# Performance work log

Hardware: AMD Instinct MI355X
Metric: run time of the kernel (lower is better)

## Reference

```python
import jax, jax.numpy as jnp
import numpy as np

NUM_HEADS = 8
SCALE_BASE = 512.0
GN_EPS = 1e-5


def rotate_every_two(x):
    x1 = x[..., ::2]
    x2 = x[..., 1::2]
    return jnp.stack([-x2, x1], axis=-1).reshape(x.shape)


def xpos_apply(x, downscale):
    # x: [B, T, D]; XPOS rotary with length-dependent scale (offset=0)
    L, D = x.shape[1], x.shape[2]
    half = D // 2
    scale_vec = (jnp.arange(0, D, 2, dtype=jnp.float32) + 0.4 * D) / (1.4 * D)  # [half]
    pos = jnp.arange(L, dtype=jnp.float32)
    scale = scale_vec[None, :] ** (pos[:, None] / SCALE_BASE)  # [L, half]
    inv_freq = 1.0 / (10000.0 ** (jnp.arange(half, dtype=jnp.float32) / half))
    sinusoid = pos[:, None] * inv_freq[None, :]  # [L, half]
    sin, cos = jnp.sin(sinusoid), jnp.cos(sinusoid)
    if downscale:
        scale = 1.0 / scale
    sin_s = jnp.repeat(sin * scale, 2, axis=-1)  # duplicate_interleave -> [L, D]
    cos_s = jnp.repeat(cos * scale, 2, axis=-1)
    return x * cos_s + rotate_every_two(x) * sin_s


def decay_mask_fn(T, num_heads):
    # gamma per head; decay stored as log(gamma) so mask = gamma^(i-j) on lower triangle
    s, e = np.log(1.0 / 32.0), np.log(1.0 / 512.0)
    gamma = 1.0 - jnp.exp(jnp.linspace(s, e, num_heads).astype(jnp.float32))
    log_decay = jnp.log(gamma)  # [H], negative
    idx = jnp.arange(T)
    expo = (idx[:, None] - idx[None, :]).astype(jnp.float32)  # i - j
    tri = (idx[:, None] >= idx[None, :])
    expo_safe = jnp.where(tri, expo, 0.0)
    mask = jnp.exp(log_decay[:, None, None] * expo_safe) * tri  # [H, T, T]
    scale = jnp.sqrt(mask.sum(axis=-1, keepdims=True))  # [H, T, 1]
    return mask / scale


def setup_inputs() -> dict:
    key = jax.random.key(0)
    ks = jax.random.split(key, 4)
    B, T, E = 2, 2048, 1024
    V = 2 * E
    return {
        "hidden_states": jax.random.normal(ks[0], (B, T, E), dtype=jnp.float32),
        "w_qkv": jax.random.normal(ks[1], (E, 2 * E + V), dtype=jnp.float32) * 0.02,
        "b_qkv": jnp.zeros((2 * E + V,), dtype=jnp.float32),
        "w_g": jax.random.normal(ks[2], (E, V), dtype=jnp.float32) * 0.02,
        "b_g": jnp.zeros((V,), dtype=jnp.float32),
        "w_p": jax.random.normal(ks[3], (V, E), dtype=jnp.float32) * 0.02,
        "b_p": jnp.zeros((E,), dtype=jnp.float32),
    }


def reference(hidden_states, w_qkv, b_qkv, w_g, b_g, w_p, b_p):
    B, T, E = hidden_states.shape
    H = NUM_HEADS
    V = 2 * E
    dk, dv = E // H, V // H

    qkv = hidden_states @ w_qkv + b_qkv
    q, k, v = qkv[..., :E], qkv[..., E:2 * E], qkv[..., 2 * E:]
    q = xpos_apply(q, downscale=False)
    k = xpos_apply(k, downscale=True)

    # split heads -> [B, H, T, d]
    q = q.reshape(B, T, H, dk).transpose(0, 2, 1, 3)
    k = k.reshape(B, T, H, dk).transpose(0, 2, 1, 3)
    v = v.reshape(B, T, H, dv).transpose(0, 2, 1, 3)

    mask = decay_mask_fn(T, H)  # [H, T, T]

    # parallel retention
    retention = jnp.einsum("bhid,bhjd->bhij", q, k) * (dk ** -0.5)
    retention = retention * mask[None]  # [B, H, T, T]
    out = jnp.einsum("bhij,bhjv->bhiv", retention, v)

    # current_kv = sum_j mask[h, -1, j] * k_j (x) v_j
    curr_kv = jnp.einsum("hj,bhjk,bhjv->bhkv", mask[:, -1, :], k, v)

    retention_out = out.transpose(0, 2, 1, 3).reshape(B, T, V)

    # GroupNorm(num_groups=H, affine=False) over v_dim channels
    g = retention_out.reshape(B * T, H, dv)
    mu = g.mean(axis=-1, keepdims=True)
    var = ((g - mu) ** 2).mean(axis=-1, keepdims=True)
    normed = ((g - mu) / jnp.sqrt(var + GN_EPS)).reshape(B, T, V)

    gated = jax.nn.silu(hidden_states @ w_g + b_g) * normed
    proj = gated @ w_p + b_p
    return proj, curr_kv
```

## Files before the change

### kernel.cpp

```cpp
#include <hip/hip_runtime.h>
#include <math.h>

#define BT      4096
#define T_SEQ   2048
#define E_DIM   1024
#define V_DIM   2048
#define DK      128
#define DV      256

typedef unsigned short ushort_t;
typedef __attribute__((ext_vector_type(8)))  short bf16x8;
typedef __attribute__((ext_vector_type(4)))  unsigned short u16x4;
typedef __attribute__((ext_vector_type(16))) float f32x16;

__device__ __forceinline__ void decay_params(int h, float& ld, float& gamma) {
    const float s0 = -3.4657359027997265f;
    const float e0 = -6.2383246250395092f;
    float lin = s0 + (e0 - s0) * ((float)h * (1.0f / 7.0f));
    gamma = 1.0f - expf(lin);
    ld = logf(gamma);
}

__device__ __forceinline__ short f2bf(float f) {
    unsigned u = __float_as_uint(f);
    unsigned r = (u + 0x7fffu + ((u >> 16) & 1u)) >> 16;
    return (short)r;
}
__device__ __forceinline__ float bf2f(ushort_t u) {
    return __uint_as_float((unsigned)u << 16);
}

__device__ __forceinline__ void async_copy16(void* lds, const void* g) {
    __builtin_amdgcn_global_load_lds(
        (const __attribute__((address_space(1))) unsigned int*)g,
        (__attribute__((address_space(3))) unsigned int*)lds, 16, 0, 0);
}

__device__ __forceinline__ void xcd_tile(int& bx, int& by) {
    const int nwgx = gridDim.x;
    const int nwg  = nwgx * gridDim.y;
    int bid = blockIdx.y * nwgx + blockIdx.x;
    bid = (bid & 7) * (nwg >> 3) + (bid >> 3);
    bx = bid % nwgx;
    by = bid / nwgx;
}

__device__ __forceinline__ void xcd_map_qkv(int& bx, int& by) {
    int bid = blockIdx.y * 16 + blockIdx.x;
    const int xcd = bid & 7, idx = bid >> 3;
    bx = (xcd & 1) * 8 + (idx & 7);
    by = (xcd >> 1) * 4 + (idx >> 3);
}

__device__ __forceinline__ void xcd_map_gate(int& bx, int& by) {
    int bid = blockIdx.y * 8 + blockIdx.x;
    const int xcd = bid & 7, idx = bid >> 3;
    bx = (xcd & 1) * 4 + (idx & 3);
    by = (xcd >> 1) * 8 + (idx >> 2);
}

__device__ __forceinline__ void transpose_tile_body(
    const float* __restrict__ W, ushort_t* __restrict__ Wt,
    int K, int N, int bx, int by, float (*tile)[33], int t)
{
    const int k0 = by * 32, n0 = bx * 32;
    const int r = t >> 3, c = (t & 7) * 4;
    float4 v = *(const float4*)&W[(size_t)(k0 + r) * N + n0 + c];
    tile[r][c] = v.x; tile[r][c + 1] = v.y; tile[r][c + 2] = v.z; tile[r][c + 3] = v.w;
    __syncthreads();
    u16x4 o;
    o[0] = (ushort_t)f2bf(tile[c][r]);
    o[1] = (ushort_t)f2bf(tile[c + 1][r]);
    o[2] = (ushort_t)f2bf(tile[c + 2][r]);
    o[3] = (ushort_t)f2bf(tile[c + 3][r]);
    *(u16x4*)&Wt[(size_t)(n0 + r) * K + k0 + c] = o;
}

__global__ __launch_bounds__(256)
void prep_batch(const float* __restrict__ hs, ushort_t* __restrict__ hs_bf,
                const float* __restrict__ w_qkv, ushort_t* __restrict__ wqkv_t,
                const float* __restrict__ w_g, ushort_t* __restrict__ wg_t)
{
    __shared__ float tile[32][33];
    const int t = threadIdx.x;
    const int blk = blockIdx.x;
    if (blk < 4096) {
        transpose_tile_body(w_qkv, wqkv_t, 1024, 4096, blk % 128, blk / 128, tile, t);
    } else if (blk < 6144) {
        const int u = blk - 4096;
        transpose_tile_body(w_g, wg_t, 1024, 2048, u % 64, u / 64, tile, t);
    } else {
        const int u = blk - 6144;
        int i = (u * 256 + t) * 8;
        float4 a = *(const float4*)&hs[i];
        float4 b = *(const float4*)&hs[i + 4];
        bf16x8 o;
        o[0] = f2bf(a.x); o[1] = f2bf(a.y); o[2] = f2bf(a.z); o[3] = f2bf(a.w);
        o[4] = f2bf(b.x); o[5] = f2bf(b.y); o[6] = f2bf(b.z); o[7] = f2bf(b.w);
        *(bf16x8*)&hs_bf[i] = o;
    }
}

__global__ __launch_bounds__(256)
void transpose_w_kernel(const float* __restrict__ W, ushort_t* __restrict__ Wt,
                        int K, int N)
{
    __shared__ float tile[32][33];
    transpose_tile_body(W, Wt, K, N, blockIdx.x, blockIdx.y, tile, threadIdx.x);
}

__global__ __launch_bounds__(512, 2)
void gemm256p8(const ushort_t* __restrict__ A,
               const ushort_t* __restrict__ Bt,
               const float* __restrict__ bias,
               ushort_t* __restrict__ C, int ldc, int nkt)
{
    __shared__ ushort_t As[2 * 16384];
    __shared__ ushort_t Bs[2 * 16384];

    const int tid = threadIdx.x;
    const int wid = tid >> 6, l = tid & 63;
    const int lc = l & 31, q = l >> 5;
    const int wr = wid >> 2, wc = wid & 3;
    int bx, by; xcd_map_qkv(bx, by);
    const int m0 = by * 256, n0 = bx * 256;

    const int sra = tid >> 3;
    const int spa = (tid & 7) ^ (sra & 7);
    const ushort_t* gA = A + (size_t)(m0 + sra) * 1024 + spa * 8;
    const int srb = tid >> 2;
    const int spb = (tid & 3) ^ ((srb >> 1) & 3);
    const ushort_t* gB = Bt + (size_t)(n0 + srb) * 1024 + spb * 8;
    const int da = tid * 8;

    int arow0 = (wr * 128 +  0 + lc) * 64;
    int arow1 = (wr * 128 + 32 + lc) * 64;
    int arow2 = (wr * 128 + 64 + lc) * 64;
    int arow3 = (wr * 128 + 96 + lc) * 64;
    int sk0 = ((0 * 2 + q) ^ (lc & 7)) * 8;
    int sk1 = ((1 * 2 + q) ^ (lc & 7)) * 8;
    int sk2 = ((2 * 2 + q) ^ (lc & 7)) * 8;
    int sk3 = ((3 * 2 + q) ^ (lc & 7)) * 8;
    int brow0 = (wc * 64 +  0 + lc) * 32;
    int brow1 = (wc * 64 + 32 + lc) * 32;
    int tk0 = ((0 + q) ^ ((lc >> 1) & 3)) * 8;
    int tk1 = ((2 + q) ^ ((lc >> 1) & 3)) * 8;
    int tk2 = 8192 + ((0 + q) ^ ((lc >> 1) & 3)) * 8;
    int tk3 = 8192 + ((2 + q) ^ ((lc >> 1) & 3)) * 8;

    f32x16 acc[4][2];
    #pragma unroll
    for (int mi = 0; mi < 4; ++mi)
        #pragma unroll
        for (int ni = 0; ni < 2; ++ni)
            #pragma unroll
            for (int e = 0; e < 16; ++e) acc[mi][ni][e] = 0.0f;

    async_copy16(&As[da],          gA);
    async_copy16(&As[8192 + da],   gA + 131072);
    async_copy16(&Bs[da],          gB);
    async_copy16(&Bs[4096 + da],   gB + 131072);
    async_copy16(&As[4096 + da],   gA + 65536);
    async_copy16(&As[12288 + da],  gA + 196608);
    async_copy16(&Bs[8192 + da],   gB + 32);
    async_copy16(&Bs[12288 + da],  gB + 131072 + 32);
    gA += 64; gB += 64;
    asm volatile("s_waitcnt vmcnt(0)" ::: "memory");
    __builtin_amdgcn_s_barrier();

    int cur = 0;
    for (int t = 0; t < nkt - 1; ++t) {
        const int cb = cur * 16384;
        const int nb = 16384 - cb;
        bf16x8 a00 = *(const bf16x8*)&As[cb + arow0 + sk0];
        bf16x8 a01 = *(const bf16x8*)&As[cb + arow0 + sk1];
        bf16x8 a10 = *(const bf16x8*)&As[cb + arow1 + sk0];
        bf16x8 a11 = *(const bf16x8*)&As[cb + arow1 + sk1];
        bf16x8 b00 = *(const bf16x8*)&Bs[cb + brow0 + tk0];
        bf16x8 b01 = *(const bf16x8*)&Bs[cb + brow0 + tk1];
        bf16x8 b10 = *(const bf16x8*)&Bs[cb + brow1 + tk0];
        bf16x8 b11 = *(const bf16x8*)&Bs[cb + brow1 + tk1];
        async_copy16(&As[nb + da],        gA);
        async_copy16(&As[nb + 8192 + da], gA + 131072);
        async_copy16(&Bs[nb + da],        gB);
        async_copy16(&Bs[nb + 4096 + da], gB + 131072);
        __builtin_amdgcn_s_barrier();
        asm volatile("s_waitcnt lgkmcnt(0)" ::: "memory");
        __builtin_amdgcn_s_setprio(1);
        acc[0][0] = __builtin_amdgcn_mfma_f32_32x32x16_bf16(a00, b00, acc[0][0], 0, 0, 0);
        acc[0][1] = __builtin_amdgcn_mfma_f32_32x32x16_bf16(a00, b10, acc[0][1], 0, 0, 0);
        acc[1][0] = __builtin_amdgcn_mfma_f32_32x32x16_bf16(a10, b00, acc[1][0], 0, 0, 0);
        acc[1][1] = __builtin_amdgcn_mfma_f32_32x32x16_bf16(a10, b10, acc[1][1], 0, 0, 0);
        acc[0][0] = __builtin_amdgcn_mfma_f32_32x32x16_bf16(a01, b01, acc[0][0], 0, 0, 0);
        acc[0][1] = __builtin_amdgcn_mfma_f32_32x32x16_bf16(a01, b11, acc[0][1], 0, 0, 0);
        acc[1][0] = __builtin_amdgcn_mfma_f32_32x32x16_bf16(a11, b01, acc[1][0], 0, 0, 0);
        acc[1][1] = __builtin_amdgcn_mfma_f32_32x32x16_bf16(a11, b11, acc[1][1], 0, 0, 0);
        __builtin_amdgcn_s_setprio(0);
        asm volatile("s_waitcnt vmcnt(6)" ::: "memory");
        __builtin_amdgcn_s_barrier();
        bf16x8 a20 = *(const bf16x8*)&As[cb + arow2 + sk0];
        bf16x8 a21 = *(const bf16x8*)&As[cb + arow2 + sk1];
        bf16x8 a30 = *(const bf16x8*)&As[cb + arow3 + sk0];
        bf16x8 a31 = *(const bf16x8*)&As[cb + arow3 + sk1];
        async_copy16(&As[nb + 4096 + da],  gA + 65536);
        async_copy16(&As[nb + 12288 + da], gA + 196608);
        __builtin_amdgcn_s_barrier();
        asm volatile("s_waitcnt lgkmcnt(0)" ::: "memory");
        __builtin_amdgcn_s_setprio(1);
        acc[2][0] = __builtin_amdgcn_mfma_f32_32x32x16_bf16(a20, b00, acc[2][0], 0, 0, 0);
        acc[2][1] = __builtin_amdgcn_mfma_f32_32x32x16_bf16(a20, b10, acc[2][1], 0, 0, 0);
        acc[3][0] = __builtin_amdgcn_mfma_f32_32x32x16_bf16(a30, b00, acc[3][0], 0, 0, 0);
        acc[3][1] = __builtin_amdgcn_mfma_f32_32x32x16_bf16(a30, b10, acc[3][1], 0, 0, 0);
        acc[2][0] = __builtin_amdgcn_mfma_f32_32x32x16_bf16(a21, b01, acc[2][0], 0, 0, 0);
        acc[2][1] = __builtin_amdgcn_mfma_f32_32x32x16_bf16(a21, b11, acc[2][1], 0, 0, 0);
        acc[3][0] = __builtin_amdgcn_mfma_f32_32x32x16_bf16(a31, b01, acc[3][0], 0, 0, 0);
        acc[3][1] = __builtin_amdgcn_mfma_f32_32x32x16_bf16(a31, b11, acc[3][1], 0, 0, 0);
        __builtin_amdgcn_s_setprio(0);
        asm volatile("s_waitcnt vmcnt(6)" ::: "memory");
        __builtin_amdgcn_s_barrier();
        bf16x8 a02 = *(const bf16x8*)&As[cb + arow0 + sk2];
        bf16x8 a03 = *(const bf16x8*)&As[cb + arow0 + sk3];
        bf16x8 a12 = *(const bf16x8*)&As[cb + arow1 + sk2];
        bf16x8 a13 = *(const bf16x8*)&As[cb + arow1 + sk3];
        bf16x8 b02 = *(const bf16x8*)&Bs[cb + brow0 + tk2];
        bf16x8 b03 = *(const bf16x8*)&Bs[cb + brow0 + tk3];
        bf16x8 b12 = *(const bf16x8*)&Bs[cb + brow1 + tk2];
        bf16x8 b13 = *(const bf16x8*)&Bs[cb + brow1 + tk3];
        async_copy16(&Bs[nb + 8192 + da],  gB + 32);
        async_copy16(&Bs[nb + 12288 + da], gB + 131072 + 32);
        gA += 64; gB += 64;
        __builtin_amdgcn_s_barrier();
        asm volatile("s_waitcnt lgkmcnt(0)" ::: "memory");
        __builtin_amdgcn_s_setprio(1);
        acc[0][0] = __builtin_amdgcn_mfma_f32_32x32x16_bf16(a02, b02, acc[0][0], 0, 0, 0);
        acc[0][1] = __builtin_amdgcn_mfma_f32_32x32x16_bf16(a02, b12, acc[0][1], 0, 0, 0);
        acc[1][0] = __builtin_amdgcn_mfma_f32_32x32x16_bf16(a12, b02, acc[1][0], 0, 0, 0);
        acc[1][1] = __builtin_amdgcn_mfma_f32_32x32x16_bf16(a12, b12, acc[1][1], 0, 0, 0);
        acc[0][0] = __builtin_amdgcn_mfma_f32_32x32x16_bf16(a03, b03, acc[0][0], 0, 0, 0);
        acc[0][1] = __builtin_amdgcn_mfma_f32_32x32x16_bf16(a03, b13, acc[0][1], 0, 0, 0);
        acc[1][0] = __builtin_amdgcn_mfma_f32_32x32x16_bf16(a13, b03, acc[1][0], 0, 0, 0);
        acc[1][1] = __builtin_amdgcn_mfma_f32_32x32x16_bf16(a13, b13, acc[1][1], 0, 0, 0);
        __builtin_amdgcn_s_setprio(0);
        __builtin_amdgcn_s_barrier();
        bf16x8 a22 = *(const bf16x8*)&As[cb + arow2 + sk2];
        bf16x8 a23 = *(const bf16x8*)&As[cb + arow2 + sk3];
        bf16x8 a32 = *(const bf16x8*)&As[cb + arow3 + sk2];
        bf16x8 a33 = *(const bf16x8*)&As[cb + arow3 + sk3];
        __builtin_amdgcn_s_barrier();
        asm volatile("s_waitcnt lgkmcnt(0)" ::: "memory");
        __builtin_amdgcn_s_setprio(1);
        acc[2][0] = __builtin_amdgcn_mfma_f32_32x32x16_bf16(a22, b02, acc[2][0], 0, 0, 0);
        acc[2][1] = __builtin_amdgcn_mfma_f32_32x32x16_bf16(a22, b12, acc[2][1], 0, 0, 0);
        acc[3][0] = __builtin_amdgcn_mfma_f32_32x32x16_bf16(a32, b02, acc[3][0], 0, 0, 0);
        acc[3][1] = __builtin_amdgcn_mfma_f32_32x32x16_bf16(a32, b12, acc[3][1], 0, 0, 0);
        acc[2][0] = __builtin_amdgcn_mfma_f32_32x32x16_bf16(a23, b03, acc[2][0], 0, 0, 0);
        acc[2][1] = __builtin_amdgcn_mfma_f32_32x32x16_bf16(a23, b13, acc[2][1], 0, 0, 0);
        acc[3][0] = __builtin_amdgcn_mfma_f32_32x32x16_bf16(a33, b03, acc[3][0], 0, 0, 0);
        acc[3][1] = __builtin_amdgcn_mfma_f32_32x32x16_bf16(a33, b13, acc[3][1], 0, 0, 0);
        __builtin_amdgcn_s_setprio(0);
        asm volatile("s_waitcnt vmcnt(4)" ::: "memory");
        __builtin_amdgcn_s_barrier();
        cur ^= 1;
    }

    {
        const int cb = cur * 16384;
        bf16x8 a00 = *(const bf16x8*)&As[cb + arow0 + sk0];
        bf16x8 a01 = *(const bf16x8*)&As[cb + arow0 + sk1];
        bf16x8 a10 = *(const bf16x8*)&As[cb + arow1 + sk0];
        bf16x8 a11 = *(const bf16x8*)&As[cb + arow1 + sk1];
        bf16x8 b00 = *(const bf16x8*)&Bs[cb + brow0 + tk0];
        bf16x8 b01 = *(const bf16x8*)&Bs[cb + brow0 + tk1];
        bf16x8 b10 = *(const bf16x8*)&Bs[cb + brow1 + tk0];
        bf16x8 b11 = *(const bf16x8*)&Bs[cb + brow1 + tk1];
        __builtin_amdgcn_s_barrier();
        asm volatile("s_waitcnt lgkmcnt(0)" ::: "memory");
        __builtin_amdgcn_s_setprio(1);
        acc[0][0] = __builtin_amdgcn_mfma_f32_32x32x16_bf16(a00, b00, acc[0][0], 0, 0, 0);
        acc[0][1] = __builtin_amdgcn_mfma_f32_32x32x16_bf16(a00, b10, acc[0][1], 0, 0, 0);
        acc[1][0] = __builtin_amdgcn_mfma_f32_32x32x16_bf16(a10, b00, acc[1][0], 0, 0, 0);
        acc[1][1] = __builtin_amdgcn_mfma_f32_32x32x16_bf16(a10, b10, acc[1][1], 0, 0, 0);
        acc[0][0] = __builtin_amdgcn_mfma_f32_32x32x16_bf16(a01, b01, acc[0][0], 0, 0, 0);
        acc[0][1] = __builtin_amdgcn_mfma_f32_32x32x16_bf16(a01, b11, acc[0][1], 0, 0, 0);
        acc[1][0] = __builtin_amdgcn_mfma_f32_32x32x16_bf16(a11, b01, acc[1][0], 0, 0, 0);
        acc[1][1] = __builtin_amdgcn_mfma_f32_32x32x16_bf16(a11, b11, acc[1][1], 0, 0, 0);
        __builtin_amdgcn_s_setprio(0);
        asm volatile("s_waitcnt vmcnt(2)" ::: "memory");
        __builtin_amdgcn_s_barrier();
        bf16x8 a20 = *(const bf16x8*)&As[cb + arow2 + sk0];
        bf16x8 a21 = *(const bf16x8*)&As[cb + arow2 + sk1];
        bf16x8 a30 = *(const bf16x8*)&As[cb + arow3 + sk0];
        bf16x8 a31 = *(const bf16x8*)&As[cb + arow3 + sk1];
        __builtin_amdgcn_s_barrier();
        asm volatile("s_waitcnt lgkmcnt(0)" ::: "memory");
        __builtin_amdgcn_s_setprio(1);
        acc[2][0] = __builtin_amdgcn_mfma_f32_32x32x16_bf16(a20, b00, acc[2][0], 0, 0, 0);
        acc[2][1] = __builtin_amdgcn_mfma_f32_32x32x16_bf16(a20, b10, acc[2][1], 0, 0, 0);
        acc[3][0] = __builtin_amdgcn_mfma_f32_32x32x16_bf16(a30, b00, acc[3][0], 0, 0, 0);
        acc[3][1] = __builtin_amdgcn_mfma_f32_32x32x16_bf16(a30, b10, acc[3][1], 0, 0, 0);
        acc[2][0] = __builtin_amdgcn_mfma_f32_32x32x16_bf16(a21, b01, acc[2][0], 0, 0, 0);
        acc[2][1] = __builtin_amdgcn_mfma_f32_32x32x16_bf16(a21, b11, acc[2][1], 0, 0, 0);
        acc[3][0] = __builtin_amdgcn_mfma_f32_32x32x16_bf16(a31, b01, acc[3][0], 0, 0, 0);
        acc[3][1] = __builtin_amdgcn_mfma_f32_32x32x16_bf16(a31, b11, acc[3][1], 0, 0, 0);
        __builtin_amdgcn_s_setprio(0);
        asm volatile("s_waitcnt vmcnt(0)" ::: "memory");
        __builtin_amdgcn_s_barrier();
        bf16x8 a02 = *(const bf16x8*)&As[cb + arow0 + sk2];
        bf16x8 a03 = *(const bf16x8*)&As[cb + arow0 + sk3];
        bf16x8 a12 = *(const bf16x8*)&As[cb + arow1 + sk2];
        bf16x8 a13 = *(const bf16x8*)&As[cb + arow1 + sk3];
        bf16x8 b02 = *(const bf16x8*)&Bs[cb + brow0 + tk2];
        bf16x8 b03 = *(const bf16x8*)&Bs[cb + brow0 + tk3];
        bf16x8 b12 = *(const bf16x8*)&Bs[cb + brow1 + tk2];
        bf16x8 b13 = *(const bf16x8*)&Bs[cb + brow1 + tk3];
        __builtin_amdgcn_s_barrier();
        asm volatile("s_waitcnt lgkmcnt(0)" ::: "memory");
        __builtin_amdgcn_s_setprio(1);
        acc[0][0] = __builtin_amdgcn_mfma_f32_32x32x16_bf16(a02, b02, acc[0][0], 0, 0, 0);
        acc[0][1] = __builtin_amdgcn_mfma_f32_32x32x16_bf16(a02, b12, acc[0][1], 0, 0, 0);
        acc[1][0] = __builtin_amdgcn_mfma_f32_32x32x16_bf16(a12, b02, acc[1][0], 0, 0, 0);
        acc[1][1] = __builtin_amdgcn_mfma_f32_32x32x16_bf16(a12, b12, acc[1][1], 0, 0, 0);
        acc[0][0] = __builtin_amdgcn_mfma_f32_32x32x16_bf16(a03, b03, acc[0][0], 0, 0, 0);
        acc[0][1] = __builtin_amdgcn_mfma_f32_32x32x16_bf16(a03, b13, acc[0][1], 0, 0, 0);
        acc[1][0] = __builtin_amdgcn_mfma_f32_32x32x16_bf16(a13, b03, acc[1][0], 0, 0, 0);
        acc[1][1] = __builtin_amdgcn_mfma_f32_32x32x16_bf16(a13, b13, acc[1][1], 0, 0, 0);
        __builtin_amdgcn_s_setprio(0);
        __builtin_amdgcn_s_barrier();
        bf16x8 a22 = *(const bf16x8*)&As[cb + arow2 + sk2];
        bf16x8 a23 = *(const bf16x8*)&As[cb + arow2 + sk3];
        bf16x8 a32 = *(const bf16x8*)&As[cb + arow3 + sk2];
        bf16x8 a33 = *(const bf16x8*)&As[cb + arow3 + sk3];
        asm volatile("s_waitcnt lgkmcnt(0)" ::: "memory");
        __builtin_amdgcn_s_setprio(1);
        acc[2][0] = __builtin_amdgcn_mfma_f32_32x32x16_bf16(a22, b02, acc[2][0], 0, 0, 0);
        acc[2][1] = __builtin_amdgcn_mfma_f32_32x32x16_bf16(a22, b12, acc[2][1], 0, 0, 0);
        acc[3][0] = __builtin_amdgcn_mfma_f32_32x32x16_bf16(a32, b02, acc[3][0], 0, 0, 0);
        acc[3][1] = __builtin_amdgcn_mfma_f32_32x32x16_bf16(a32, b12, acc[3][1], 0, 0, 0);
        acc[2][0] = __builtin_amdgcn_mfma_f32_32x32x16_bf16(a23, b03, acc[2][0], 0, 0, 0);
        acc[2][1] = __builtin_amdgcn_mfma_f32_32x32x16_bf16(a23, b13, acc[2][1], 0, 0, 0);
        acc[3][0] = __builtin_amdgcn_mfma_f32_32x32x16_bf16(a33, b03, acc[3][0], 0, 0, 0);
        acc[3][1] = __builtin_amdgcn_mfma_f32_32x32x16_bf16(a33, b13, acc[3][1], 0, 0, 0);
        __builtin_amdgcn_s_setprio(0);
    }

    {
        const float bb0 = bias[n0 + wc * 64 + lc];
        const float bb1 = bias[n0 + wc * 64 + 32 + lc];
        #pragma unroll
        for (int mi = 0; mi < 4; ++mi) {
            #pragma unroll
            for (int r = 0; r < 16; ++r) {
                const int row = m0 + wr * 128 + mi * 32 + (r & 3) + 8 * (r >> 2) + 4 * q;
                ushort_t* cp = C + (size_t)row * ldc + n0 + wc * 64 + lc;
                cp[0]  = (ushort_t)f2bf(acc[mi][0][r] + bb0);
                cp[32] = (ushort_t)f2bf(acc[mi][1][r] + bb1);
            }
        }
    }
}

__global__ __launch_bounds__(512)
void gemm_gate_p8(const ushort_t* __restrict__ A,
                  const ushort_t* __restrict__ Bt,
                  const float* __restrict__ bias,
                  ushort_t* __restrict__ C, int ldc,
                  int nkt)
{
    __shared__ ushort_t As[2 * 8192];
    __shared__ ushort_t Bs[2 * 16384];

    const int tid = threadIdx.x;
    const int wid = tid >> 6, l = tid & 63;
    const int lc = l & 31, q = l >> 5;
    const int wr = wid >> 2, wc = wid & 3;
    int bx, by; xcd_map_gate(bx, by);
    const int m0 = by * 128, n0 = bx * 256;

    const int sra = tid >> 3;
    const int spa = (tid & 7) ^ (sra & 7);
    const ushort_t* gA = A + (size_t)(m0 + sra) * 1024 + spa * 8;
    const int srb = tid >> 2;
    const int spb = (tid & 3) ^ ((srb >> 1) & 3);
    const ushort_t* gB = Bt + (size_t)(n0 + srb) * 1024 + spb * 8;
    const int da = tid * 8;

    int arow0 = (wr * 64 +  0 + lc) * 64;
    int arow1 = (wr * 64 + 32 + lc) * 64;
    int sk0 = ((0 * 2 + q) ^ (lc & 7)) * 8;
    int sk1 = ((1 * 2 + q) ^ (lc & 7)) * 8;
    int sk2 = ((2 * 2 + q) ^ (lc & 7)) * 8;
    int sk3 = ((3 * 2 + q) ^ (lc & 7)) * 8;
    int brow0 = (wc * 64 +  0 + lc) * 32;
    int brow1 = (wc * 64 + 32 + lc) * 32;
    int tk0 = ((0 + q) ^ ((lc >> 1) & 3)) * 8;
    int tk1 = ((2 + q) ^ ((lc >> 1) & 3)) * 8;
    int tk2 = 8192 + ((0 + q) ^ ((lc >> 1) & 3)) * 8;
    int tk3 = 8192 + ((2 + q) ^ ((lc >> 1) & 3)) * 8;

    f32x16 acc[2][2];
    #pragma unroll
    for (int mi = 0; mi < 2; ++mi)
        #pragma unroll
        for (int ni = 0; ni < 2; ++ni)
            #pragma unroll
            for (int e = 0; e < 16; ++e) acc[mi][ni][e] = 0.0f;

    async_copy16(&As[da],          gA);
    async_copy16(&As[4096 + da],   gA + 65536);
    async_copy16(&Bs[da],          gB);
    async_copy16(&Bs[4096 + da],   gB + 131072);
    async_copy16(&Bs[8192 + da],   gB + 32);
    async_copy16(&Bs[12288 + da],  gB + 131072 + 32);
    gA += 64; gB += 64;
    asm volatile("s_waitcnt vmcnt(0)" ::: "memory");
    __builtin_amdgcn_s_barrier();

    int cur = 0;
    for (int t = 0; t < nkt - 1; ++t) {
        const int ca = cur * 8192,  na = 8192 - ca;
        const int cb = cur * 16384, nb = 16384 - cb;
        bf16x8 a00 = *(const bf16x8*)&As[ca + arow0 + sk0];
        bf16x8 a01 = *(const bf16x8*)&As[ca + arow0 + sk1];
        bf16x8 a10 = *(const bf16x8*)&As[ca + arow1 + sk0];
        bf16x8 a11 = *(const bf16x8*)&As[ca + arow1 + sk1];
        bf16x8 b00 = *(const bf16x8*)&Bs[cb + brow0 + tk0];
        bf16x8 b01 = *(const bf16x8*)&Bs[cb + brow0 + tk1];
        bf16x8 b10 = *(const bf16x8*)&Bs[cb + brow1 + tk0];
        bf16x8 b11 = *(const bf16x8*)&Bs[cb + brow1 + tk1];
        async_copy16(&As[na + da],        gA);
        async_copy16(&As[na + 4096 + da], gA + 65536);
        async_copy16(&Bs[nb + da],        gB);
        async_copy16(&Bs[nb + 4096 + da], gB + 131072);
        __builtin_amdgcn_s_barrier();
        asm volatile("s_waitcnt lgkmcnt(0)" ::: "memory");
        __builtin_amdgcn_s_setprio(1);
        acc[0][0] = __builtin_amdgcn_mfma_f32_32x32x16_bf16(a00, b00, acc[0][0], 0, 0, 0);
        acc[0][1] = __builtin_amdgcn_mfma_f32_32x32x16_bf16(a00, b10, acc[0][1], 0, 0, 0);
        acc[1][0] = __builtin_amdgcn_mfma_f32_32x32x16_bf16(a10, b00, acc[1][0], 0, 0, 0);
        acc[1][1] = __builtin_amdgcn_mfma_f32_32x32x16_bf16(a10, b10, acc[1][1], 0, 0, 0);
        acc[0][0] = __builtin_amdgcn_mfma_f32_32x32x16_bf16(a01, b01, acc[0][0], 0, 0, 0);
        acc[0][1] = __builtin_amdgcn_mfma_f32_32x32x16_bf16(a01, b11, acc[0][1], 0, 0, 0);
        acc[1][0] = __builtin_amdgcn_mfma_f32_32x32x16_bf16(a11, b01, acc[1][0], 0, 0, 0);
        acc[1][1] = __builtin_amdgcn_mfma_f32_32x32x16_bf16(a11, b11, acc[1][1], 0, 0, 0);
        __builtin_amdgcn_s_setprio(0);
        asm volatile("s_waitcnt vmcnt(4)" ::: "memory");
        __builtin_amdgcn_s_barrier();
        bf16x8 a02 = *(const bf16x8*)&As[ca + arow0 + sk2];
        bf16x8 a03 = *(const bf16x8*)&As[ca + arow0 + sk3];
        bf16x8 a12 = *(const bf16x8*)&As[ca + arow1 + sk2];
        bf16x8 a13 = *(const bf16x8*)&As[ca + arow1 + sk3];
        bf16x8 b02 = *(const bf16x8*)&Bs[cb + brow0 + tk2];
        bf16x8 b03 = *(const bf16x8*)&Bs[cb + brow0 + tk3];
        bf16x8 b12 = *(const bf16x8*)&Bs[cb + brow1 + tk2];
        bf16x8 b13 = *(const bf16x8*)&Bs[cb + brow1 + tk3];
        async_copy16(&Bs[nb + 8192 + da],  gB + 32);
        async_copy16(&Bs[nb + 12288 + da], gB + 131072 + 32);
        gA += 64; gB += 64;
        __builtin_amdgcn_s_barrier();
        asm volatile("s_waitcnt lgkmcnt(0)" ::: "memory");
        __builtin_amdgcn_s_setprio(1);
        acc[0][0] = __builtin_amdgcn_mfma_f32_32x32x16_bf16(a02, b02, acc[0][0], 0, 0, 0);
        acc[0][1] = __builtin_amdgcn_mfma_f32_32x32x16_bf16(a02, b12, acc[0][1], 0, 0, 0);
        acc[1][0] = __builtin_amdgcn_mfma_f32_32x32x16_bf16(a12, b02, acc[1][0], 0, 0, 0);
        acc[1][1] = __builtin_amdgcn_mfma_f32_32x32x16_bf16(a12, b12, acc[1][1], 0, 0, 0);
        acc[0][0] = __builtin_amdgcn_mfma_f32_32x32x16_bf16(a03, b03, acc[0][0], 0, 0, 0);
        acc[0][1] = __builtin_amdgcn_mfma_f32_32x32x16_bf16(a03, b13, acc[0][1], 0, 0, 0);
        acc[1][0] = __builtin_amdgcn_mfma_f32_32x32x16_bf16(a13, b03, acc[1][0], 0, 0, 0);
        acc[1][1] = __builtin_amdgcn_mfma_f32_32x32x16_bf16(a13, b13, acc[1][1], 0, 0, 0);
        __builtin_amdgcn_s_setprio(0);
        asm volatile("s_waitcnt vmcnt(2)" ::: "memory");
        __builtin_amdgcn_s_barrier();
        cur ^= 1;
    }

    {
        const int ca = cur * 8192;
        const int cb = cur * 16384;
        bf16x8 a00 = *(const bf16x8*)&As[ca + arow0 + sk0];
        bf16x8 a01 = *(const bf16x8*)&As[ca + arow0 + sk1];
        bf16x8 a10 = *(const bf16x8*)&As[ca + arow1 + sk0];
        bf16x8 a11 = *(const bf16x8*)&As[ca + arow1 + sk1];
        bf16x8 b00 = *(const bf16x8*)&Bs[cb + brow0 + tk0];
        bf16x8 b01 = *(const bf16x8*)&Bs[cb + brow0 + tk1];
        bf16x8 b10 = *(const bf16x8*)&Bs[cb + brow1 + tk0];
        bf16x8 b11 = *(const bf16x8*)&Bs[cb + brow1 + tk1];
        __builtin_amdgcn_s_barrier();
        asm volatile("s_waitcnt lgkmcnt(0)" ::: "memory");
        __builtin_amdgcn_s_setprio(1);
        acc[0][0] = __builtin_amdgcn_mfma_f32_32x32x16_bf16(a00, b00, acc[0][0], 0, 0, 0);
        acc[0][1] = __builtin_amdgcn_mfma_f32_32x32x16_bf16(a00, b10, acc[0][1], 0, 0, 0);
        acc[1][0] = __builtin_amdgcn_mfma_f32_32x32x16_bf16(a10, b00, acc[1][0], 0, 0, 0);
        acc[1][1] = __builtin_amdgcn_mfma_f32_32x32x16_bf16(a10, b10, acc[1][1], 0, 0, 0);
        acc[0][0] = __builtin_amdgcn_mfma_f32_32x32x16_bf16(a01, b01, acc[0][0], 0, 0, 0);
        acc[0][1] = __builtin_amdgcn_mfma_f32_32x32x16_bf16(a01, b11, acc[0][1], 0, 0, 0);
        acc[1][0] = __builtin_amdgcn_mfma_f32_32x32x16_bf16(a11, b01, acc[1][0], 0, 0, 0);
        acc[1][1] = __builtin_amdgcn_mfma_f32_32x32x16_bf16(a11, b11, acc[1][1], 0, 0, 0);
        __builtin_amdgcn_s_setprio(0);
        asm volatile("s_waitcnt vmcnt(0)" ::: "memory");
        __builtin_amdgcn_s_barrier();
        bf16x8 a02 = *(const bf16x8*)&As[ca + arow0 + sk2];
        bf16x8 a03 = *(const bf16x8*)&As[ca + arow0 + sk3];
        bf16x8 a12 = *(const bf16x8*)&As[ca + arow1 + sk2];
        bf16x8 a13 = *(const bf16x8*)&As[ca + arow1 + sk3];
        bf16x8 b02 = *(const bf16x8*)&Bs[cb + brow0 + tk2];
        bf16x8 b03 = *(const bf16x8*)&Bs[cb + brow0 + tk3];
        bf16x8 b12 = *(const bf16x8*)&Bs[cb + brow1 + tk2];
        bf16x8 b13 = *(const bf16x8*)&Bs[cb + brow1 + tk3];
        asm volatile("s_waitcnt lgkmcnt(0)" ::: "memory");
        __builtin_amdgcn_s_setprio(1);
        acc[0][0] = __builtin_amdgcn_mfma_f32_32x32x16_bf16(a02, b02, acc[0][0], 0, 0, 0);
        acc[0][1] = __builtin_amdgcn_mfma_f32_32x32x16_bf16(a02, b12, acc[0][1], 0, 0, 0);
        acc[1][0] = __builtin_amdgcn_mfma_f32_32x32x16_bf16(a12, b02, acc[1][0], 0, 0, 0);
        acc[1][1] = __builtin_amdgcn_mfma_f32_32x32x16_bf16(a12, b12, acc[1][1], 0, 0, 0);
        acc[0][0] = __builtin_amdgcn_mfma_f32_32x32x16_bf16(a03, b03, acc[0][0], 0, 0, 0);
        acc[0][1] = __builtin_amdgcn_mfma_f32_32x32x16_bf16(a03, b13, acc[0][1], 0, 0, 0);
        acc[1][0] = __builtin_amdgcn_mfma_f32_32x32x16_bf16(a13, b03, acc[1][0], 0, 0, 0);
        acc[1][1] = __builtin_amdgcn_mfma_f32_32x32x16_bf16(a13, b13, acc[1][1], 0, 0, 0);
        __builtin_amdgcn_s_setprio(0);
    }

    {
        const float bb0 = bias[n0 + wc * 64 + lc];
        const float bb1 = bias[n0 + wc * 64 + 32 + lc];
        #pragma unroll
        for (int mi = 0; mi < 2; ++mi) {
            #pragma unroll
            for (int r = 0; r < 16; ++r) {
                const int row = m0 + wr * 64 + mi * 32 + (r & 3) + 8 * (r >> 2) + 4 * q;
                ushort_t* cp = C + (size_t)row * ldc + n0 + wc * 64 + lc;
                float v0 = acc[mi][0][r] + bb0;
                float v1 = acc[mi][1][r] + bb1;
                cp[0]  = (ushort_t)f2bf(v0 / (1.0f + expf(-v0)));
                cp[32] = (ushort_t)f2bf(v1 / (1.0f + expf(-v1)));
            }
        }
    }
}

__global__ __launch_bounds__(256)
void gemm_tm64(const ushort_t* __restrict__ A, int lda,
               const ushort_t* __restrict__ Bt, int ldb,
               const float* __restrict__ bias,
               float* __restrict__ C, int ldc, int nkt)
{
    __shared__ ushort_t As[3 * 64 * 32];
    __shared__ ushort_t Bs[3 * 128 * 32];

    const int tid = threadIdx.x;
    const int w  = tid >> 6, l = tid & 63;
    const int lc = l & 31, q = l >> 5;
    const int wr = w >> 1, wc = w & 1;
    int bx, by; xcd_tile(bx, by);
    const int m0 = by * 64, n0 = bx * 128;

    const int rA = tid >> 2,          kcA = (tid & 3) ^ ((rA >> 1) & 3);
    const int rB1 = (256 + tid) >> 2, kcB1 = (tid & 3) ^ ((rB1 >> 1) & 3);
    const ushort_t* gA  = A  + (size_t)(m0 + rA)  * lda + kcA  * 8;
    const ushort_t* gB0 = Bt + (size_t)(n0 + rA)  * ldb + kcA  * 8;
    const ushort_t* gB1 = Bt + (size_t)(n0 + rB1) * ldb + kcB1 * 8;
    const int sA  = w * 512;
    const int sB0 = w * 512;
    const int sB1 = 2048 + w * 512;

    const int sl = (lc >> 1) & 3;
    int aoff[2], boff[2][2];
    #pragma unroll
    for (int ks = 0; ks < 2; ++ks) {
        const int kk = ks * 2 + q;
        const int mrow = wr * 32 + lc;
        aoff[ks] = (mrow * 4 + (kk ^ sl)) * 8;
        #pragma unroll
        for (int ni = 0; ni < 2; ++ni) {
            const int nrow = wc * 64 + ni * 32 + lc;
            boff[ni][ks] = (nrow * 4 + (kk ^ sl)) * 8;
        }
    }

    f32x16 acc[2];
    #pragma unroll
    for (int ni = 0; ni < 2; ++ni)
        #pragma unroll
        for (int e = 0; e < 16; ++e) acc[ni][e] = 0.0f;

    auto stage = [&](int ab, int bb) {
        async_copy16(&As[ab + sA], gA);
        async_copy16(&Bs[bb + sB0], gB0); async_copy16(&Bs[bb + sB1], gB1);
        gA += 32; gB0 += 32; gB1 += 32;
    };
    auto compute = [&](int ab, int bb) {
        bf16x8 a[2], b[2][2];
        #pragma unroll
        for (int ks = 0; ks < 2; ++ks) {
            a[ks] = *(const bf16x8*)&As[ab + aoff[ks]];
            b[0][ks] = *(const bf16x8*)&Bs[bb + boff[0][ks]];
            b[1][ks] = *(const bf16x8*)&Bs[bb + boff[1][ks]];
        }
        #pragma unroll
        for (int ks = 0; ks < 2; ++ks)
            #pragma unroll
            for (int ni = 0; ni < 2; ++ni)
                acc[ni] = __builtin_amdgcn_mfma_f32_32x32x16_bf16(
                    a[ks], b[ni][ks], acc[ni], 0, 0, 0);
    };

    stage(0, 0); stage(2048, 4096);
    int as_ = 4096, bs_ = 8192;
    int ac_ = 0,    bc_ = 0;
    for (int kt = 0; kt < nkt - 2; ++kt) {
        asm volatile("s_waitcnt vmcnt(3)" ::: "memory");
        __builtin_amdgcn_s_barrier();
        stage(as_, bs_);
        compute(ac_, bc_);
        as_ = ac_; bs_ = bc_;
        ac_ = (ac_ == 4096) ? 0 : ac_ + 2048;
        bc_ = (bc_ == 8192) ? 0 : bc_ + 4096;
    }
    asm volatile("s_waitcnt vmcnt(3)" ::: "memory");
    __builtin_amdgcn_s_barrier();
    compute(ac_, bc_);
    ac_ = (ac_ == 4096) ? 0 : ac_ + 2048;
    bc_ = (bc_ == 8192) ? 0 : bc_ + 4096;
    asm volatile("s_waitcnt vmcnt(0)" ::: "memory");
    __builtin_amdgcn_s_barrier();
    compute(ac_, bc_);

    #pragma unroll
    for (int ni = 0; ni < 2; ++ni) {
        const int col = n0 + wc * 64 + ni * 32 + lc;
        const float bb = bias[col];
        #pragma unroll
        for (int r = 0; r < 16; ++r) {
            const int row = m0 + wr * 32 + (r & 3) + 8 * (r >> 2) + 4 * q;
            C[(size_t)row * ldc + col] = acc[ni][r] + bb;
        }
    }
}

__global__ __launch_bounds__(256)
void qkv_prep(const ushort_t* __restrict__ qkvb,
              ushort_t* __restrict__ qh, ushort_t* __restrict__ kh,
              ushort_t* __restrict__ vt)
{
    __shared__ ushort_t tile[32][40];
    const int blk = blockIdx.x;
    const int t = threadIdx.x;
    if (blk < 4096) {
        const int row = blk;
        const int b = row >> 11, trow = row & (T_SEQ - 1);
        const bool isK = t >= 128;
        const int col0 = (t & 127) * 8;
        const int h = col0 >> 7, d = col0 & 127;

        float ld, gamma;
        decay_params(h, ld, gamma);
        const float gsc = __expf(isK ? -ld * (float)(trow & 63) : ld * (float)(trow & 63));

        const ushort_t* src = qkvb + (size_t)row * 4096 + (isK ? E_DIM : 0) + col0;
        bf16x8 xv8 = *(const bf16x8*)src;
        float xv[8];
        #pragma unroll
        for (int p = 0; p < 8; ++p) xv[p] = bf2f((ushort_t)xv8[p]);

        const float tf = (float)trow * (1.0f / 512.0f);
        bf16x8 o;
        #pragma unroll
        for (int pi = 0; pi < 4; ++pi) {
            const int ip = col0 / 2 + pi;
            float sv = (2.0f * (float)ip + 409.6f) * (1.0f / 1433.6f);
            float e = __logf(sv) * tf;
            if (isK) e = -e;
            float sc = __expf(e);
            float invf = __expf((float)ip * -0.017988946038999563f);
            float sn, cs;
            sincosf((float)trow * invf, &sn, &cs);
            float c = cs * sc * gsc, s = sn * sc * gsc;
            float a = xv[2 * pi], bb = xv[2 * pi + 1];
            o[2 * pi]     = f2bf(a * c - bb * s);
            o[2 * pi + 1] = f2bf(bb * c + a * s);
        }
        ushort_t* dst = (isK ? kh : qh) + ((size_t)(b * 8 + h) * T_SEQ + trow) * 128 + d;
        *(bf16x8*)dst = o;
    } else {
        const int u = blk - 4096;
        const int j0 = (u & 63) * 32;
        const int zz = u >> 6;
        const int bh = zz >> 3, v0 = (zz & 7) * 32;
        const int b = bh >> 3, h = bh & 7;
        const int r = t >> 3, c = (t & 7) * 4;

        *(u16x4*)&tile[r][c] = *(const u16x4*)(qkvb + (size_t)(b * T_SEQ + j0 + r) * 4096
                                               + 2 * E_DIM + h * DV + v0 + c);
        __syncthreads();
        u16x4 o;
        o[0] = tile[c][r];
        o[1] = tile[c + 1][r];
        o[2] = tile[c + 2][r];
        o[3] = tile[c + 3][r];
        *(u16x4*)&vt[((size_t)bh * 256 + v0 + r) * T_SEQ + j0 + c] = o;
    }
}

__global__ __launch_bounds__(256)
void kt2_kernel(const ushort_t* __restrict__ kh, ushort_t* __restrict__ kt2)
{
    __shared__ ushort_t tile[32][40];
    const int j0 = blockIdx.x * 32;
    const int zz = blockIdx.y;
    const int bh = zz >> 2, k0 = (zz & 3) * 32;
    const int t = threadIdx.x;
    const int r = t >> 3, c = (t & 7) * 4;
    float ld, gamma; decay_params(bh & 7, ld, gamma);
    const float g63 = expf(ld * 63.0f);
    *(u16x4*)&tile[r][c] = *(const u16x4*)&kh[((size_t)bh * T_SEQ + j0 + r) * 128 + k0 + c];
    __syncthreads();
    u16x4 o;
    o[0] = (ushort_t)f2bf(bf2f(tile[c][r])     * g63);
    o[1] = (ushort_t)f2bf(bf2f(tile[c + 1][r]) * g63);
    o[2] = (ushort_t)f2bf(bf2f(tile[c + 2][r]) * g63);
    o[3] = (ushort_t)f2bf(bf2f(tile[c + 3][r]) * g63);
    *(u16x4*)&kt2[((size_t)bh * 128 + k0 + r) * T_SEQ + j0 + c] = o;
}

__global__ __launch_bounds__(256)
void chunk_kv(const ushort_t* __restrict__ vt, const ushort_t* __restrict__ kt2,
              ushort_t* __restrict__ Abuf)
{
    const int c = blockIdx.x;
    const int bh = blockIdx.y;
    const int tid = threadIdx.x;
    const int w = tid >> 6, l = tid & 63, lc = l & 31, q = l >> 5;
    const int j0 = c * 64;

    f32x16 acc[2][4];
    #pragma unroll
    for (int mi = 0; mi < 2; ++mi)
        #pragma unroll
        for (int ni = 0; ni < 4; ++ni)
            #pragma unroll
            for (int e = 0; e < 16; ++e) acc[mi][ni][e] = 0.0f;

    #pragma unroll
    for (int ks = 0; ks < 4; ++ks) {
        bf16x8 a[2], bfr[4];
        #pragma unroll
        for (int mi = 0; mi < 2; ++mi)
            a[mi] = *(const bf16x8*)(vt + ((size_t)bh * 256 + w * 64 + mi * 32 + lc) * T_SEQ
                                     + j0 + ks * 16 + q * 8);
        #pragma unroll
        for (int ni = 0; ni < 4; ++ni)
            bfr[ni] = *(const bf16x8*)(kt2 + ((size_t)bh * 128 + ni * 32 + lc) * T_SEQ
                                       + j0 + ks * 16 + q * 8);
        #pragma unroll
        for (int mi = 0; mi < 2; ++mi)
            #pragma unroll
            for (int ni = 0; ni < 4; ++ni)
                acc[mi][ni] = __builtin_amdgcn_mfma_f32_32x32x16_bf16(
                    a[mi], bfr[ni], acc[mi][ni], 0, 0, 0);
    }

    ushort_t* ab = Abuf + (size_t)(bh * 32 + c) * 256 * 128;
    #pragma unroll
    for (int mi = 0; mi < 2; ++mi)
        #pragma unroll
        for (int ni = 0; ni < 4; ++ni)
            #pragma unroll
            for (int r = 0; r < 16; ++r) {
                const int v = w * 64 + mi * 32 + (r & 3) + 8 * (r >> 2) + 4 * q;
                const int k = ni * 32 + lc;
                ab[(size_t)v * 128 + k] = (ushort_t)f2bf(acc[mi][ni][r]);
            }
}

__global__ __launch_bounds__(256)
void scan_state(const ushort_t* Abuf, ushort_t* St,
                float* __restrict__ ckv)
{
    const int blk = blockIdx.x;
    const int bh = blk >> 7, sub = blk & 127;
    const int tid = threadIdx.x;
    const int v = sub * 2 + (tid >> 7), k = tid & 127;

    float ld, gamma;
    decay_params(bh & 7, ld, gamma);
    const float g64 = expf(ld * 64.0f);

    const size_t base = ((size_t)bh * 32 * 256 + v) * 128 + k;
    const size_t cstr = 256 * 128;
    float s = 0.0f;
    for (int c = 0; c < 32; ++c) {
        const size_t off = base + (size_t)c * cstr;
        const float a = bf2f(Abuf[off]);
        St[off] = (ushort_t)f2bf(gamma * s);
        s = g64 * s + a;
    }
    const float inv_scale = rsqrtf((1.0f - expf(ld * (float)T_SEQ)) / (1.0f - gamma));
    ckv[((size_t)bh * 128 + k) * 256 + v] = s * inv_scale;
}

__global__ __launch_bounds__(64)
void retention_chunk(const ushort_t* __restrict__ qh,
                     const ushort_t* __restrict__ kh,
                     const ushort_t* __restrict__ vt,
                     const ushort_t* __restrict__ St,
                     const ushort_t* __restrict__ grw,
                     ushort_t* __restrict__ gated)
{
    const int it = blockIdx.x;
    const int bh = blockIdx.y;
    const int b = bh >> 3, h = bh & 7;
    const int c = it >> 1, w = it & 1;
    const int l = threadIdx.x, lc = l & 31, q = l >> 5;
    const int i0 = it * 32;
    const size_t bhT = (size_t)bh * T_SEQ;

    float ld, gamma;
    decay_params(h, ld, gamma);

    bf16x8 qf[8];
    {
        const ushort_t* qp = qh + (bhT + i0 + lc) * 128 + q * 8;
        #pragma unroll
        for (int c8 = 0; c8 < 8; ++c8)
            qf[c8] = *(const bf16x8*)(qp + c8 * 16);
    }

    f32x16 acc[8];
    #pragma unroll
    for (int vg = 0; vg < 8; ++vg)
        #pragma unroll
        for (int e = 0; e < 16; ++e) acc[vg][e] = 0.0f;

    if (c > 0) {
        const ushort_t* sp = St + ((size_t)(bh * 32 + c) * 256 + lc) * 128 + q * 8;
        #pragma unroll
        for (int vg = 0; vg < 8; ++vg) {
            const ushort_t* spv = sp + (size_t)vg * 32 * 128;
            #pragma unroll
            for (int ks = 0; ks < 8; ++ks) {
                bf16x8 sb = *(const bf16x8*)(spv + ks * 16);
                acc[vg] = __builtin_amdgcn_mfma_f32_32x32x16_bf16(
                    qf[ks], sb, acc[vg], 0, 0, 0);
            }
        }
    }

    for (int jt2 = 0; jt2 <= w; ++jt2) {
        const int j0 = c * 64 + jt2 * 32;

        f32x16 s;
        #pragma unroll
        for (int e = 0; e < 16; ++e) s[e] = 0.0f;
        const ushort_t* kp = kh + (bhT + j0 + lc) * 128 + q * 8;
        #pragma unroll
        for (int c8 = 0; c8 < 8; ++c8) {
            bf16x8 ka = *(const bf16x8*)(kp + c8 * 16);
            s = __builtin_amdgcn_mfma_f32_32x32x16_bf16(ka, qf[c8], s, 0, 0, 0);
        }

        float sv[16];
        #pragma unroll
        for (int r = 0; r < 16; ++r) {
            float val = s[r];
            if (jt2 == w) {
                int jr_ = (r & 3) + 8 * (r >> 2) + 4 * q;
                val = (jr_ <= lc) ? val : 0.0f;
            }
            sv[r] = val;
        }

        bf16x8 pa0, pa1;
        #pragma unroll
        for (int e = 0; e < 4; ++e) {
            float t1 = __shfl_xor(sv[e + 4], 32);
            float t0 = __shfl_xor(sv[e], 32);
            pa0[e]     = f2bf(q ? t1 : sv[e]);
            pa0[e + 4] = f2bf(q ? sv[e + 4] : t0);
            float t3 = __shfl_xor(sv[e + 12], 32);
            float t2 = __shfl_xor(sv[e + 8], 32);
            pa1[e]     = f2bf(q ? t3 : sv[e + 8]);
            pa1[e + 4] = f2bf(q ? sv[e + 12] : t2);
        }

        #pragma unroll
        for (int vg = 0; vg < 8; ++vg) {
            const ushort_t* vp = vt + ((size_t)bh * 256 + vg * 32 + lc) * T_SEQ + j0 + q * 8;
            bf16x8 vb0 = *(const bf16x8*)vp;
            bf16x8 vb1 = *(const bf16x8*)(vp + 16);
            acc[vg] = __builtin_amdgcn_mfma_f32_32x32x16_bf16(pa0, vb0, acc[vg], 0, 0, 0);
            acc[vg] = __builtin_amdgcn_mfma_f32_32x32x16_bf16(pa1, vb1, acc[vg], 0, 0, 0);
        }
    }

    #pragma unroll
    for (int r = 0; r < 16; ++r) {
        const int il = (r & 3) + 8 * (r >> 2) + 4 * q;
        const int i  = i0 + il;
        float denom = (1.0f - expf(ld * (float)(i + 1))) / (1.0f - gamma);
        float fs = 0.08838834764831845f * rsqrtf(denom);
        float vals[8];
        float a1 = 0.0f, a2 = 0.0f;
        #pragma unroll
        for (int vg = 0; vg < 8; ++vg) {
            float x = acc[vg][r] * fs;
            vals[vg] = x;
            a1 += x; a2 += x * x;
        }
        a1 += __shfl_xor(a1, 1);  a2 += __shfl_xor(a2, 1);
        a1 += __shfl_xor(a1, 2);  a2 += __shfl_xor(a2, 2);
        a1 += __shfl_xor(a1, 4);  a2 += __shfl_xor(a2, 4);
        a1 += __shfl_xor(a1, 8);  a2 += __shfl_xor(a2, 8);
        a1 += __shfl_xor(a1, 16); a2 += __shfl_xor(a2, 16);
        float mu = a1 * (1.0f / 256.0f);
        float var = a2 * (1.0f / 256.0f) - mu * mu;
        float rs = rsqrtf(var + 1e-5f);
        const size_t ob = ((size_t)(b * T_SEQ + i)) * V_DIM + h * DV + lc;
        ushort_t* op = gated + ob;
        const ushort_t* gp = grw + ob;
        #pragma unroll
        for (int vg = 0; vg < 8; ++vg) {
            float g = bf2f(gp[vg * 32]);
            op[vg * 32] = (ushort_t)f2bf((vals[vg] - mu) * rs * g);
        }
    }
}

extern "C" void kernel_launch(void* const* d_in, const int* in_sizes, int n_in,
                              void* d_out, int out_size, void* d_ws, size_t ws_size,
                              hipStream_t stream)
{
    const float* hs    = (const float*)d_in[0];
    const float* w_qkv = (const float*)d_in[1];
    const float* b_qkv = (const float*)d_in[2];
    const float* w_g   = (const float*)d_in[3];
    const float* b_g   = (const float*)d_in[4];
    const float* w_p   = (const float*)d_in[5];
    const float* b_p   = (const float*)d_in[6];
    float* out = (float*)d_out;

    const size_t MB = 1024 * 1024;
    ushort_t* qkv_bf   = (ushort_t*)d_ws;
    ushort_t* Abuf     = (ushort_t*)d_ws;
    ushort_t* Stbuf    = (ushort_t*)d_ws;
    ushort_t* wp_t     = (ushort_t*)d_ws;
    ushort_t* gate_raw = (ushort_t*)((char*)d_ws + 32 * MB);
    ushort_t* gated_bf = (ushort_t*)((char*)d_ws + 48 * MB);
    ushort_t* wg_t     = (ushort_t*)((char*)d_ws + 64 * MB);
    ushort_t* qh       = (ushort_t*)((char*)d_ws + 64 * MB);
    ushort_t* vt       = (ushort_t*)((char*)d_ws + 72 * MB);
    ushort_t* wqkv_t   = (ushort_t*)((char*)d_ws + 88 * MB);
    ushort_t* kh       = (ushort_t*)((char*)d_ws + 88 * MB);
    ushort_t* hs_bf    = (ushort_t*)d_out;
    ushort_t* kt2      = (ushort_t*)((char*)d_out + 8 * MB);
    float*    ckv_out  = out + (size_t)BT * E_DIM;

    prep_batch<<<dim3(8192), 256, 0, stream>>>(hs, hs_bf, w_qkv, wqkv_t, w_g, wg_t);

    gemm_gate_p8<<<dim3(8, 32), 512, 0, stream>>>(
        hs_bf, wg_t, b_g, gate_raw, V_DIM, E_DIM / 64);

    gemm256p8<<<dim3(16, 16), 512, 0, stream>>>(
        hs_bf, wqkv_t, b_qkv, qkv_bf, 4096, E_DIM / 64);

    qkv_prep<<<dim3(12288), 256, 0, stream>>>(qkv_bf, qh, kh, vt);
    kt2_kernel<<<dim3(64, 64), 256, 0, stream>>>(kh, kt2);

    chunk_kv<<<dim3(32, 16), 256, 0, stream>>>(vt, kt2, Abuf);
    scan_state<<<dim3(2048), 256, 0, stream>>>(Abuf, Stbuf, ckv_out);
    retention_chunk<<<dim3(64, 16), 64, 0, stream>>>(qh, kh, vt, Stbuf, gate_raw, gated_bf);

    transpose_w_kernel<<<dim3(32, 64), 256, 0, stream>>>(w_p, wp_t, V_DIM, E_DIM);
    gemm_tm64<<<dim3(8, 64), 256, 0, stream>>>(
        gated_bf, V_DIM, wp_t, V_DIM, b_p, out, E_DIM, V_DIM / 32);
}
```

Before: 295.6 us.

## Split retention_chunk V dimension across two waves with LDS GroupNorm reduction

The retention_chunk kernel now launches 128 threads per block, and each wave computes half of the 256 value columns (4 of 8 MFMA accumulator groups). The GroupNorm partial sums are exchanged between the two waves through shared memory and a barrier. This doubles the wave count, halves per-wave accumulator registers and MFMA work to improve occupancy and latency hiding. In exchange, both waves redundantly recompute the QK^T score tile and load the Q fragments, and a block sync is added.

```diff
diff --git a/kernel.cpp b/kernel.cpp
--- a/kernel.cpp
+++ b/kernel.cpp
@@ -797,7 +797,7 @@
     ckv[((size_t)bh * 128 + k) * 256 + v] = s * inv_scale;
 }
 
-__global__ __launch_bounds__(64)
+__global__ __launch_bounds__(128)
 void retention_chunk(const ushort_t* __restrict__ qh,
                      const ushort_t* __restrict__ kh,
                      const ushort_t* __restrict__ vt,
@@ -805,11 +805,16 @@
                      const ushort_t* __restrict__ grw,
                      ushort_t* __restrict__ gated)
 {
+    __shared__ float red[2][2][16][2];
+
     const int it = blockIdx.x;
     const int bh = blockIdx.y;
     const int b = bh >> 3, h = bh & 7;
     const int c = it >> 1, w = it & 1;
-    const int l = threadIdx.x, lc = l & 31, q = l >> 5;
+    const int tid = threadIdx.x;
+    const int wv = tid >> 6;
+    const int l = tid & 63, lc = l & 31, q = l >> 5;
+    const int vg0 = wv * 4;
     const int i0 = it * 32;
     const size_t bhT = (size_t)bh * T_SEQ;
 
@@ -824,16 +829,16 @@
             qf[c8] = *(const bf16x8*)(qp + c8 * 16);
     }
 
-    f32x16 acc[8];
-    #pragma unroll
-    for (int vg = 0; vg < 8; ++vg)
+    f32x16 acc[4];
+    #pragma unroll
+    for (int vg = 0; vg < 4; ++vg)
         #pragma unroll
         for (int e = 0; e < 16; ++e) acc[vg][e] = 0.0f;
 
     if (c > 0) {
-        const ushort_t* sp = St + ((size_t)(bh * 32 + c) * 256 + lc) * 128 + q * 8;
-        #pragma unroll
-        for (int vg = 0; vg < 8; ++vg) {
+        const ushort_t* sp = St + ((size_t)(bh * 32 + c) * 256 + vg0 * 32 + lc) * 128 + q * 8;
+        #pragma unroll
+        for (int vg = 0; vg < 4; ++vg) {
             const ushort_t* spv = sp + (size_t)vg * 32 * 128;
             #pragma unroll
             for (int ks = 0; ks < 8; ++ks) {
@@ -882,8 +887,9 @@
         }
 
         #pragma unroll
-        for (int vg = 0; vg < 8; ++vg) {
-            const ushort_t* vp = vt + ((size_t)bh * 256 + vg * 32 + lc) * T_SEQ + j0 + q * 8;
+        for (int vg = 0; vg < 4; ++vg) {
+            const ushort_t* vp = vt + ((size_t)bh * 256 + (vg0 + vg) * 32 + lc) * T_SEQ
+                                 + j0 + q * 8;
             bf16x8 vb0 = *(const bf16x8*)vp;
             bf16x8 vb1 = *(const bf16x8*)(vp + 16);
             acc[vg] = __builtin_amdgcn_mfma_f32_32x32x16_bf16(pa0, vb0, acc[vg], 0, 0, 0);
@@ -891,18 +897,17 @@
         }
     }
 
+    float fsv[16], p1[16], p2[16];
     #pragma unroll
     for (int r = 0; r < 16; ++r) {
         const int il = (r & 3) + 8 * (r >> 2) + 4 * q;
         const int i  = i0 + il;
         float denom = (1.0f - expf(ld * (float)(i + 1))) / (1.0f - gamma);
-        float fs = 0.08838834764831845f * rsqrtf(denom);
-        float vals[8];
+        fsv[r] = 0.08838834764831845f * rsqrtf(denom);
         float a1 = 0.0f, a2 = 0.0f;
         #pragma unroll
-        for (int vg = 0; vg < 8; ++vg) {
-            float x = acc[vg][r] * fs;
-            vals[vg] = x;
+        for (int vg = 0; vg < 4; ++vg) {
+            float x = acc[vg][r] * fsv[r];
             a1 += x; a2 += x * x;
         }
         a1 += __shfl_xor(a1, 1);  a2 += __shfl_xor(a2, 1);
@@ -910,6 +915,23 @@
         a1 += __shfl_xor(a1, 4);  a2 += __shfl_xor(a2, 4);
         a1 += __shfl_xor(a1, 8);  a2 += __shfl_xor(a2, 8);
         a1 += __shfl_xor(a1, 16); a2 += __shfl_xor(a2, 16);
+        p1[r] = a1; p2[r] = a2;
+    }
+    if (lc == 0) {
+        #pragma unroll
+        for (int r = 0; r < 16; ++r) {
+            red[wv][q][r][0] = p1[r];
+            red[wv][q][r][1] = p2[r];
+        }
+    }
+    __syncthreads();
+
+    #pragma unroll
+    for (int r = 0; r < 16; ++r) {
+        const int il = (r & 3) + 8 * (r >> 2) + 4 * q;
+        const int i  = i0 + il;
+        float a1 = p1[r] + red[1 - wv][q][r][0];
+        float a2 = p2[r] + red[1 - wv][q][r][1];
         float mu = a1 * (1.0f / 256.0f);
         float var = a2 * (1.0f / 256.0f) - mu * mu;
         float rs = rsqrtf(var + 1e-5f);
@@ -917,9 +939,10 @@
         ushort_t* op = gated + ob;
         const ushort_t* gp = grw + ob;
         #pragma unroll
-        for (int vg = 0; vg < 8; ++vg) {
-            float g = bf2f(gp[vg * 32]);
-            op[vg * 32] = (ushort_t)f2bf((vals[vg] - mu) * rs * g);
+        for (int vg = 0; vg < 4; ++vg) {
+            float x = acc[vg][r] * fsv[r];
+            float g = bf2f(gp[(vg0 + vg) * 32]);
+            op[(vg0 + vg) * 32] = (ushort_t)f2bf((x - mu) * rs * g);
         }
     }
 }
@@ -966,7 +989,7 @@
 
     chunk_kv<<<dim3(32, 16), 256, 0, stream>>>(vt, kt2, Abuf);
     scan_state<<<dim3(2048), 256, 0, stream>>>(Abuf, Stbuf, ckv_out);
-    retention_chunk<<<dim3(64, 16), 64, 0, stream>>>(qh, kh, vt, Stbuf, gate_raw, gated_bf);
+    retention_chunk<<<dim3(64, 16), 128, 0, stream>>>(qh, kh, vt, Stbuf, gate_raw, gated_bf);
 
     transpose_w_kernel<<<dim3(32, 64), 256, 0, stream>>>(w_p, wp_t, V_DIM, E_DIM);
     gemm_tm64<<<dim3(8, 64), 256, 0, stream>>>(
```

New measurement: 292.4 us (median of 2 runs). About the same (-1.1%).
